# Performance work log

Measured on AMD Instinct MI355X. Metric: run time of the kernel, lower is better.

Reference implementation:

```python
import jax, jax.numpy as jnp
import numpy as np

M1 = M2 = M3 = 8  # retained modes per spatial dim


def get_3d_clifford_kernel(w, g):
    # w: (8, O, I, 2m1, 2m2, 2m3); returns (8O, 8I, 2m1, 2m2, 2m3)
    g0, g1, g2 = g[0], g[1], g[2]
    k0 = jnp.concatenate([w[0], w[1] * g0, w[2] * g1, w[3] * g2, -w[4] * g0 * g1, -w[5] * g0 * g2, -w[6] * g1 * g2, -w[7] * g0 * g1 * g2], axis=1)
    k1 = jnp.concatenate([w[1], w[0], -w[4] * g1, -w[5] * g2, w[2] * g1, w[3] * g2, -w[7] * g1 * g2, -w[6] * g1 * g2], axis=1)
    k2 = jnp.concatenate([w[2], w[4] * g0, w[0], -w[6] * g2, -w[1] * g0, w[7] * g0 * g2, w[3] * g2, w[5] * g0 * g2], axis=1)
    k3 = jnp.concatenate([w[3], w[5] * g0, w[6] * g1, w[0], -w[7] * g0 * g1, -w[1] * g0, -w[2] * g1, -w[4] * g0 * g1], axis=1)
    k4 = jnp.concatenate([w[4], w[2], -w[1], g2 * w[7], w[0], -w[6] * g2, w[5] * g2, w[3] * g2], axis=1)
    k5 = jnp.concatenate([w[5], w[3], -w[7] * g1, -w[1], w[6] * g1, w[0], -w[4] * g1, -w[2] * g1], axis=1)
    k6 = jnp.concatenate([w[6], w[7] * g0, w[3], -w[2], -w[5] * g0, w[4] * g0, w[0], w[1] * g0], axis=1)
    k7 = jnp.concatenate([w[7], w[6], -w[5], w[4], w[3], -w[2], w[1], w[0]], axis=1)
    return jnp.concatenate([k0, k1, k2, k3, k4, k5, k6, k7], axis=0)


def setup_inputs() -> dict:
    key = jax.random.key(0)
    k1, k2 = jax.random.split(key)
    B, D, H, W, Cin, Cout = 4, 48, 48, 48, 24, 24
    x = jax.random.normal(k1, (B, D, H, W, Cin, 8), dtype=jnp.float32)
    scale = 1.0 / (Cin * Cout)
    weights = scale * jax.random.uniform(k2, (8, Cout, Cin, 2 * M1, 2 * M2, 2 * M3), dtype=jnp.float32)
    return {"x": x, "weights": weights}


def reference(x, weights):
    B, D, H, W, Cin, _ = x.shape
    Cout = weights.shape[1]
    g = jnp.ones(3, dtype=x.dtype)  # metric (1, 1, 1)
    # complex-dual packing of the 8 blades
    d1 = x[..., 0] + 1j * x[..., 7]
    d2 = x[..., 1] + 1j * x[..., 6]
    d3 = x[..., 2] + 1j * x[..., 5]
    d4 = x[..., 3] + 1j * x[..., 4]
    f1 = jnp.fft.fftn(d1, axes=(1, 2, 3))
    f2 = jnp.fft.fftn(d2, axes=(1, 2, 3))
    f3 = jnp.fft.fftn(d3, axes=(1, 2, 3))
    f4 = jnp.fft.fftn(d4, axes=(1, 2, 3))
    bchw = lambda t: t.transpose(0, 4, 1, 2, 3)
    # (B, 8*Cin, D, H, W) real tensor of blade spectra
    mv_ft = jnp.concatenate([bchw(f1.real), bchw(f2.real), bchw(f3.real), bchw(f4.real),
                             bchw(f4.imag), bchw(f3.imag), bchw(f2.imag), bchw(f1.imag)], axis=1)
    # gather the 8 low/high-frequency octant corners -> (B, 8Cin, 2m1, 2m2, 2m3)
    i1 = jnp.concatenate([jnp.arange(M1), jnp.arange(D - M1, D)])
    i2 = jnp.concatenate([jnp.arange(M2), jnp.arange(H - M2, H)])
    i3 = jnp.concatenate([jnp.arange(M3), jnp.arange(W - M3, W)])
    input_mul = mv_ft[:, :, i1[:, None, None], i2[None, :, None], i3[None, None, :]]
    kernel = get_3d_clifford_kernel(weights, g)  # (8Cout, 8Cin, 2m1, 2m2, 2m3)
    output_mul = jnp.einsum("bixyz,oixyz->boxyz", input_mul, kernel)
    # scatter back to full spectrum
    out_ft = jnp.zeros((B, 8 * Cout, D, H, W), dtype=mv_ft.dtype)
    out_ft = out_ft.at[:, :, i1[:, None, None], i2[None, :, None], i3[None, None, :]].set(output_mul)
    out_ft = out_ft.reshape(B, 8, Cout, D, H, W).transpose(0, 2, 3, 4, 5, 1)  # (B, Cout, D, H, W, 8)
    o1 = out_ft[..., 0] + 1j * out_ft[..., 7]
    o2 = out_ft[..., 1] + 1j * out_ft[..., 6]
    o3 = out_ft[..., 2] + 1j * out_ft[..., 5]
    o4 = out_ft[..., 3] + 1j * out_ft[..., 4]
    g1_ = jnp.fft.ifftn(o1, axes=(2, 3, 4))
    g2_ = jnp.fft.ifftn(o2, axes=(2, 3, 4))
    g3_ = jnp.fft.ifftn(o3, axes=(2, 3, 4))
    g4_ = jnp.fft.ifftn(o4, axes=(2, 3, 4))
    output = jnp.stack([g1_.real, g2_.real, g3_.real, g4_.real,
                        g4_.imag, g3_.imag, g2_.imag, g1_.imag], axis=-1)  # (B, Cout, D, H, W, 8)
    return output.transpose(0, 2, 3, 4, 1, 5)  # (B, D, H, W, Cout, 8)
```

## Files before the change

kernel.cpp:

```cpp
#include <hip/hip_runtime.h>
#include <math.h>


#define C866 0.8660254037844386f

constexpr float FC0[8] = {1.0f, 0.99144486137885f, 0.96592582628907f, 0.92387953251129f,
                          0.86602540378444f, 0.79335334029124f, 0.70710678118655f, 0.60876142900872f};
constexpr float FS0[8] = {0.0f, 0.13052619222005f, 0.25881904510252f, 0.38268343236509f,
                          0.5f, 0.60876142900872f, 0.70710678118655f, 0.79335334029124f};
constexpr float FC1[8] = {0.5f, 0.60876142900872f, 0.70710678118655f, 0.79335334029124f,
                          0.86602540378444f, 0.92387953251129f, 0.96592582628907f, 0.99144486137885f};
constexpr float FS1[8] = {-0.86602540378444f, -0.79335334029124f, -0.70710678118655f, -0.60876142900872f,
                          -0.5f, -0.38268343236509f, -0.25881904510252f, -0.13052619222005f};

__device__ __forceinline__ uint32_t c2h(float2 z) {
  union { _Float16 h[2]; uint32_t u; } v;
  v.h[0] = (_Float16)z.x; v.h[1] = (_Float16)z.y;
  return v.u;
}
__device__ __forceinline__ float2 h2c(uint32_t u) {
  union { uint32_t u; _Float16 h[2]; } v;
  v.u = u;
  return make_float2((float)v.h[0], (float)v.h[1]);
}

__device__ __forceinline__ float2 cmul(float2 a, float2 b) {
  return make_float2(fmaf(a.x, b.x, -(a.y * b.y)), fmaf(a.x, b.y, a.y * b.x));
}
__device__ __forceinline__ void cfma(float2& acc, float2 a, float2 t) {
  acc.x = fmaf(a.x, t.x, acc.x); acc.x = fmaf(-a.y, t.y, acc.x);
  acc.y = fmaf(a.x, t.y, acc.y); acc.y = fmaf(a.y, t.x, acc.y);
}

struct FwdState {
  float2 acc[8], t[8], stp[8];
  float2 R1, R2;
};

__device__ __forceinline__ void fwd_init(FwdState& st, int half) {
#pragma unroll
  for (int r = 0; r < 8; ++r) {
    st.acc[r] = make_float2(0.f, 0.f);
    st.t[r] = make_float2(1.f, 0.f);
    st.stp[r] = make_float2(half ? FC1[r] : FC0[r],
                            half ? -FS1[r] : -FS0[r]);
  }
  st.R1 = half ? make_float2(-0.5f, -C866) : make_float2(1.f, 0.f);
  st.R2 = half ? make_float2(-0.5f,  C866) : make_float2(1.f, 0.f);
}

__device__ __forceinline__ void fwd_stepf(FwdState& st, float2 z0, float2 z1, float2 z2) {
  z1 = cmul(z1, st.R1);
  z2 = cmul(z2, st.R2);
  const float sx = z1.x + z2.x, sy = z1.y + z2.y;
  const float dx = z1.x - z2.x, dy = z1.y - z2.y;
  const float2 y0 = make_float2(z0.x + sx, z0.y + sy);
  const float tx = fmaf(-0.5f, sx, z0.x), ty = fmaf(-0.5f, sy, z0.y);
  const float ex = C866 * dx, ey = C866 * dy;
  const float2 y1 = make_float2(tx + ey, ty - ex);
  const float2 y2 = make_float2(tx - ey, ty + ex);
#pragma unroll
  for (int r = 0; r < 8; ++r) {
    const float2 yy = (r % 3 == 0) ? y0 : ((r % 3 == 1) ? y1 : y2);
    cfma(st.acc[r], yy, st.t[r]);
    st.t[r] = cmul(st.t[r], st.stp[r]);
  }
}

struct InvState {
  float2 zr[16], t[16];
};

__device__ __forceinline__ void inv_init(InvState& st) {
#pragma unroll
  for (int m = 0; m < 16; ++m) st.t[m] = make_float2(1.f, 0.f);
}

__device__ __forceinline__ void inv_stepf(InvState& st, float2& o0, float2& o1, float2& o2) {
  constexpr int JG[16] = {0,1,2,0,1,2,0,1, 1,2,0,1,2,0,1,2};
  float2 u0 = make_float2(0.f, 0.f), u1 = u0, u2 = u0;
#pragma unroll
  for (int m = 0; m < 16; ++m) {
    float2& uu = (JG[m] == 0) ? u0 : ((JG[m] == 1) ? u1 : u2);
    cfma(uu, st.zr[m], st.t[m]);
    const float2 stp = (m < 8) ? make_float2(FC0[m], FS0[m])
                               : make_float2(FC1[m - 8], FS1[m - 8]);
    st.t[m] = cmul(st.t[m], stp);
  }
  const float sx = u1.x + u2.x, sy = u1.y + u2.y;
  const float dx = u1.x - u2.x, dy = u1.y - u2.y;
  o0 = make_float2(u0.x + sx, u0.y + sy);
  const float tx = fmaf(-0.5f, sx, u0.x), ty = fmaf(-0.5f, sy, u0.y);
  const float ex = C866 * dx, ey = C866 * dy;
  o1 = make_float2(tx - ey, ty + ex);
  o2 = make_float2(tx + ey, ty - ex);
}

__global__ __launch_bounds__(192) void k_fwd_w(const float* __restrict__ x,
                                               uint32_t* __restrict__ A) {
  __shared__ __align__(16) uint32_t xs[48 * 96];
  {
    const float* xp = x + (size_t)blockIdx.x * 9216;
    for (int idx = threadIdx.x; idx < 1152; idx += 192) {
      const int w = idx / 24, ci = idx % 24;
      const float4 u = *(const float4*)(xp + w * 192 + ci * 8);
      const float4 v = *(const float4*)(xp + w * 192 + ci * 8 + 4);
      uint4 d;
      d.x = c2h(make_float2(u.x, v.w));
      d.y = c2h(make_float2(u.y, v.z));
      d.z = c2h(make_float2(u.z, v.y));
      d.w = c2h(make_float2(u.w, v.x));
      *(uint4*)(&xs[w * 96 + ci * 4]) = d;
    }
  }
  __syncthreads();

  const int q = threadIdx.x % 96, half = threadIdx.x / 96;
  FwdState st;
  fwd_init(st, half);
#pragma unroll 4
  for (int j = 0; j < 16; ++j) {
    const float2 z0 = h2c(xs[j * 96 + q]);
    const float2 z1 = h2c(xs[(j + 16) * 96 + q]);
    const float2 z2 = h2c(xs[(j + 32) * 96 + q]);
    fwd_stepf(st, z0, z1, z2);
  }
  const int bd = blockIdx.x / 48, h = blockIdx.x % 48;
  uint32_t* Ap = A + (((size_t)bd * 16 + half * 8) * 48 + h) * 96 + q;
#pragma unroll
  for (int r = 0; r < 8; ++r) Ap[(size_t)r * 4608] = c2h(st.acc[r]);
}

__global__ __launch_bounds__(192) void k_fwd_h(const uint32_t* __restrict__ A,
                                               uint32_t* __restrict__ Bv) {
  const int k3 = blockIdx.x & 15, bd = blockIdx.x >> 4;
  const int q = threadIdx.x % 96, half = threadIdx.x / 96;
  const uint32_t* Ap = A + ((size_t)bd * 16 + k3) * 4608 + q;
  FwdState st;
  fwd_init(st, half);
#pragma unroll 4
  for (int j = 0; j < 16; ++j) {
    const float2 z0 = h2c(Ap[j * 96]);
    const float2 z1 = h2c(Ap[(j + 16) * 96]);
    const float2 z2 = h2c(Ap[(j + 32) * 96]);
    fwd_stepf(st, z0, z1, z2);
  }
  const int b = bd / 48, d = bd % 48;
  uint32_t* Bp = Bv + (((size_t)b * 256 + half * 8 * 16 + k3) * 48 + d) * 96 + q;
#pragma unroll
  for (int r = 0; r < 8; ++r) Bp[(size_t)r * 73728] = c2h(st.acc[r]);
}

__global__ __launch_bounds__(192) void k_fwd_d(const uint32_t* __restrict__ Bv,
                                               uint32_t* __restrict__ Cv) {
  const int k23 = blockIdx.x & 255, b = blockIdx.x >> 8;
  const int q = threadIdx.x % 96, half = threadIdx.x / 96;
  const uint32_t* Bp = Bv + ((size_t)b * 256 + k23) * 4608 + q;
  FwdState st;
  fwd_init(st, half);
#pragma unroll 4
  for (int j = 0; j < 16; ++j) {
    const float2 z0 = h2c(Bp[j * 96]);
    const float2 z1 = h2c(Bp[(j + 16) * 96]);
    const float2 z2 = h2c(Bp[(j + 32) * 96]);
    fwd_stepf(st, z0, z1, z2);
  }
  uint32_t* Cp = Cv + ((size_t)b * 4096 + k23) * 96 + q;
#pragma unroll
  for (int r = 0; r < 8; ++r) Cp[(size_t)(half * 8 + r) * 24576] = c2h(st.acc[r]);
}

__global__ __launch_bounds__(256) void k_einsum(const uint32_t* __restrict__ Cv,
                                                const float* __restrict__ wgt,
                                                uint32_t* __restrict__ OMz) {
  const int mode = blockIdx.x * 64 + (threadIdx.x & 63);
  const int co = blockIdx.y * 4 + (threadIdx.x >> 6);
  const int cih = blockIdx.z;

  constexpr int WIDX[8][8] = {
      {0, 1, 2, 3, 4, 5, 6, 7}, {1, 0, 4, 5, 2, 3, 7, 6},
      {2, 4, 0, 6, 1, 7, 3, 5}, {3, 5, 6, 0, 7, 1, 2, 4},
      {4, 2, 1, 7, 0, 6, 5, 3}, {5, 3, 7, 1, 6, 0, 4, 2},
      {6, 7, 3, 2, 5, 4, 0, 1}, {7, 6, 5, 4, 3, 2, 1, 0}};
  constexpr int SGN[8][8] = {
      {1, 1, 1, 1, -1, -1, -1, -1}, {1, 1, -1, -1, 1, 1, -1, -1},
      {1, 1, 1, -1, -1, 1, 1, 1},   {1, 1, 1, 1, -1, -1, -1, -1},
      {1, 1, -1, 1, 1, -1, 1, 1},   {1, 1, -1, -1, 1, 1, -1, -1},
      {1, 1, 1, -1, -1, 1, 1, 1},   {1, 1, -1, 1, 1, -1, 1, 1}};

  float acc[8][4];
#pragma unroll
  for (int bo = 0; bo < 8; ++bo)
#pragma unroll
    for (int b = 0; b < 4; ++b) acc[bo][b] = 0.f;

#pragma unroll 2
  for (int cc = 0; cc < 12; ++cc) {
    const int ci = cih * 12 + cc;
    float w8[8];
#pragma unroll
    for (int k = 0; k < 8; ++k)
      w8[k] = wgt[(size_t)((k * 24 + co) * 24 + ci) * 4096 + mode];
#pragma unroll
    for (int b = 0; b < 4; ++b) {
      const uint4 U = *(const uint4*)(Cv + ((size_t)(b * 4096 + mode) * 96 + ci * 4));
      const float2 z0 = h2c(U.x), z1 = h2c(U.y), z2 = h2c(U.z), z3 = h2c(U.w);
      const float inv[8] = {z0.x, z1.x, z2.x, z3.x, z3.y, z2.y, z1.y, z0.y};
#pragma unroll
      for (int bo = 0; bo < 8; ++bo) {
#pragma unroll
        for (int bi = 0; bi < 8; ++bi) {
          const float wv = w8[WIDX[bo][bi]];
          if (SGN[bo][bi] > 0)
            acc[bo][b] = fmaf(wv, inv[bi], acc[bo][b]);
          else
            acc[bo][b] = fmaf(wv, -inv[bi], acc[bo][b]);
        }
      }
    }
  }
  uint32_t* OMp = OMz + (size_t)cih * 1572864;
#pragma unroll
  for (int b = 0; b < 4; ++b) {
    uint4 P;
    P.x = c2h(make_float2(acc[0][b], acc[7][b]));
    P.y = c2h(make_float2(acc[1][b], acc[6][b]));
    P.z = c2h(make_float2(acc[2][b], acc[5][b]));
    P.w = c2h(make_float2(acc[3][b], acc[4][b]));
    *(uint4*)(OMp + ((size_t)(b * 4096 + mode) * 96 + co * 4)) = P;
  }
}

__global__ __launch_bounds__(192) void k_inv_d(const uint32_t* __restrict__ OMz,
                                               uint32_t* __restrict__ IS1) {
  const int col = blockIdx.x * 2 + threadIdx.x / 96;
  const int q = threadIdx.x % 96;
  const int k23 = col & 255, b = col >> 8;
  const int k2 = k23 >> 4, k3 = k23 & 15;
  InvState st;
#pragma unroll
  for (int m = 0; m < 16; ++m) {
    const size_t idx = ((size_t)b * 4096 + m * 256 + k23) * 96 + q;
    const float2 pa = h2c(OMz[idx]);
    const float2 pb = h2c(OMz[idx + 1572864]);
    st.zr[m] = make_float2(pa.x + pb.x, pa.y + pb.y);
  }
  inv_init(st);
  uint32_t* Op = IS1 + ((size_t)b * 12288 + k3 * 16 + k2) * 96 + q;
#pragma unroll 2
  for (int j = 0; j < 16; ++j) {
    float2 o0, o1, o2;
    inv_stepf(st, o0, o1, o2);
    Op[(size_t)j * 24576] = c2h(o0);
    Op[(size_t)(j + 16) * 24576] = c2h(o1);
    Op[(size_t)(j + 32) * 24576] = c2h(o2);
  }
}

__global__ __launch_bounds__(192) void k_inv_h(const uint32_t* __restrict__ IS1,
                                               uint32_t* __restrict__ IS2) {
  const int col = blockIdx.x * 2 + threadIdx.x / 96;
  const int q = threadIdx.x % 96;
  const int m3 = col & 15, bd = col >> 4;
  const uint32_t* Ip = IS1 + ((size_t)bd * 256 + m3 * 16) * 96 + q;
  InvState st;
#pragma unroll
  for (int m = 0; m < 16; ++m) st.zr[m] = h2c(Ip[m * 96]);
  inv_init(st);
  uint32_t* Op = IS2 + ((size_t)bd * 768 + m3) * 96 + q;
#pragma unroll 2
  for (int j = 0; j < 16; ++j) {
    float2 o0, o1, o2;
    inv_stepf(st, o0, o1, o2);
    Op[(size_t)j * 1536] = c2h(o0);
    Op[(size_t)(j + 16) * 1536] = c2h(o1);
    Op[(size_t)(j + 32) * 1536] = c2h(o2);
  }
}

__global__ __launch_bounds__(192) void k_inv_w(const uint32_t* __restrict__ IS2,
                                               float* __restrict__ out) {
  const int blk = blockIdx.x * 2 + threadIdx.x / 96;
  const int q = threadIdx.x % 96;
  const int co = q >> 2, c = q & 3;
  const float norm = 1.0f / 110592.0f;
  InvState st;
#pragma unroll
  for (int m = 0; m < 16; ++m) {
    float2 z = h2c(IS2[((size_t)blk * 16 + m) * 96 + q]);
    st.zr[m] = make_float2(z.x * norm, z.y * norm);
  }
  inv_init(st);
  float* ob = out + (size_t)blk * 9216 + co * 8;
#pragma unroll 2
  for (int j = 0; j < 16; ++j) {
    float2 o0, o1, o2;
    inv_stepf(st, o0, o1, o2);
    float* p0 = ob + (size_t)j * 192;
    float* p1 = ob + (size_t)(j + 16) * 192;
    float* p2 = ob + (size_t)(j + 32) * 192;
    p0[c] = o0.x; p0[7 - c] = o0.y;
    p1[c] = o1.x; p1[7 - c] = o1.y;
    p2[c] = o2.x; p2[7 - c] = o2.y;
  }
}

extern "C" void kernel_launch(void* const* d_in, const int* in_sizes, int n_in,
                              void* d_out, int out_size, void* d_ws, size_t ws_size,
                              hipStream_t stream) {
  (void)in_sizes; (void)n_in; (void)out_size; (void)ws_size;
  const float* x = (const float*)d_in[0];
  const float* wgt = (const float*)d_in[1];
  float* out = (float*)d_out;

  char* ob = (char*)d_out;
  uint32_t* A   = (uint32_t*)(ob + 0);
  uint32_t* Bv  = (uint32_t*)(ob + 56623104);
  uint32_t* Cv  = (uint32_t*)(ob + 75497472);
  uint32_t* OMz = (uint32_t*)(ob + 81788928);
  uint32_t* IS1 = (uint32_t*)(ob + 0);
  uint32_t* IS2 = (uint32_t*)d_ws;

  k_fwd_w<<<9216, 192, 0, stream>>>(x, A);
  k_fwd_h<<<3072, 192, 0, stream>>>(A, Bv);
  k_fwd_d<<<1024, 192, 0, stream>>>(Bv, Cv);
  k_einsum<<<dim3(64, 6, 2), 256, 0, stream>>>(Cv, wgt, OMz);
  k_inv_d<<<512, 192, 0, stream>>>(OMz, IS1);
  k_inv_h<<<1536, 192, 0, stream>>>(IS1, IS2);
  k_inv_w<<<4608, 192, 0, stream>>>(IS2, out);
}
```

Baseline: 309.5 us.

## Fuse inverse H and W FFT passes through shared memory

Merges the inverse H-axis and W-axis FFT kernels into one kernel. The H-pass results for a (b,d) slice and a group of 24 channels are kept in LDS instead of going through a global intermediate, and the W-pass then reads them from LDS. This removes one global write/read round trip of the half-precision intermediate and one kernel launch. In exchange it uses about 75KB of LDS per block, which lowers occupancy, and the grid shrinks to 768 blocks of 384 threads. IS1 now lives in the workspace rather than the output buffer.

```diff
diff --git a/kernel.cpp b/kernel.cpp
--- a/kernel.cpp
+++ b/kernel.cpp
@@ -257,51 +257,58 @@
   }
 }
 
-__global__ __launch_bounds__(192) void k_inv_h(const uint32_t* __restrict__ IS1,
-                                               uint32_t* __restrict__ IS2) {
-  const int col = blockIdx.x * 2 + threadIdx.x / 96;
-  const int q = threadIdx.x % 96;
-  const int m3 = col & 15, bd = col >> 4;
-  const uint32_t* Ip = IS1 + ((size_t)bd * 256 + m3 * 16) * 96 + q;
-  InvState st;
-#pragma unroll
-  for (int m = 0; m < 16; ++m) st.zr[m] = h2c(Ip[m * 96]);
-  inv_init(st);
-  uint32_t* Op = IS2 + ((size_t)bd * 768 + m3) * 96 + q;
+__global__ __launch_bounds__(384) void k_inv_hw(const uint32_t* __restrict__ IS1,
+                                                float* __restrict__ out) {
+  __shared__ uint32_t sb[48 * 392];
+  const int bd = blockIdx.x, qg = blockIdx.y;
+  const int tid = threadIdx.x;
+  const int ql = tid % 24;
+  const int q = qg * 24 + ql;
+
+  {
+    const int m3 = tid / 24;
+    const uint32_t* Ip = IS1 + ((size_t)bd * 256 + m3 * 16) * 96 + q;
+    InvState st;
+#pragma unroll
+    for (int m2 = 0; m2 < 16; ++m2) st.zr[m2] = h2c(Ip[m2 * 96]);
+    inv_init(st);
+    uint32_t* sp = &sb[m3 * 24 + ql];
 #pragma unroll 2
-  for (int j = 0; j < 16; ++j) {
-    float2 o0, o1, o2;
-    inv_stepf(st, o0, o1, o2);
-    Op[(size_t)j * 1536] = c2h(o0);
-    Op[(size_t)(j + 16) * 1536] = c2h(o1);
-    Op[(size_t)(j + 32) * 1536] = c2h(o2);
-  }
-}
-
-__global__ __launch_bounds__(192) void k_inv_w(const uint32_t* __restrict__ IS2,
-                                               float* __restrict__ out) {
-  const int blk = blockIdx.x * 2 + threadIdx.x / 96;
-  const int q = threadIdx.x % 96;
-  const int co = q >> 2, c = q & 3;
-  const float norm = 1.0f / 110592.0f;
-  InvState st;
-#pragma unroll
-  for (int m = 0; m < 16; ++m) {
-    float2 z = h2c(IS2[((size_t)blk * 16 + m) * 96 + q]);
-    st.zr[m] = make_float2(z.x * norm, z.y * norm);
-  }
-  inv_init(st);
-  float* ob = out + (size_t)blk * 9216 + co * 8;
+    for (int j = 0; j < 16; ++j) {
+      float2 o0, o1, o2;
+      inv_stepf(st, o0, o1, o2);
+      sp[(size_t)j * 392] = c2h(o0);
+      sp[(size_t)(j + 16) * 392] = c2h(o1);
+      sp[(size_t)(j + 32) * 392] = c2h(o2);
+    }
+  }
+  __syncthreads();
+  {
+    const int co = q >> 2, c = q & 3;
+    const float norm = 1.0f / 110592.0f;
+    for (int hh = 0; hh < 3; ++hh) {
+      const int h = hh * 16 + tid / 24;
+      const uint32_t* sp = &sb[h * 392 + ql];
+      InvState st;
+#pragma unroll
+      for (int m3 = 0; m3 < 16; ++m3) {
+        const float2 z = h2c(sp[m3 * 24]);
+        st.zr[m3] = make_float2(z.x * norm, z.y * norm);
+      }
+      inv_init(st);
+      float* ob = out + (((size_t)bd * 48 + h) * 48) * 192 + co * 8;
 #pragma unroll 2
-  for (int j = 0; j < 16; ++j) {
-    float2 o0, o1, o2;
-    inv_stepf(st, o0, o1, o2);
-    float* p0 = ob + (size_t)j * 192;
-    float* p1 = ob + (size_t)(j + 16) * 192;
-    float* p2 = ob + (size_t)(j + 32) * 192;
-    p0[c] = o0.x; p0[7 - c] = o0.y;
-    p1[c] = o1.x; p1[7 - c] = o1.y;
-    p2[c] = o2.x; p2[7 - c] = o2.y;
+      for (int j = 0; j < 16; ++j) {
+        float2 o0, o1, o2;
+        inv_stepf(st, o0, o1, o2);
+        float* p0 = ob + (size_t)j * 192;
+        float* p1 = ob + (size_t)(j + 16) * 192;
+        float* p2 = ob + (size_t)(j + 32) * 192;
+        p0[c] = o0.x; p0[7 - c] = o0.y;
+        p1[c] = o1.x; p1[7 - c] = o1.y;
+        p2[c] = o2.x; p2[7 - c] = o2.y;
+      }
+    }
   }
 }
 
@@ -318,14 +325,12 @@
   uint32_t* Bv  = (uint32_t*)(ob + 56623104);
   uint32_t* Cv  = (uint32_t*)(ob + 75497472);
   uint32_t* OMz = (uint32_t*)(ob + 81788928);
-  uint32_t* IS1 = (uint32_t*)(ob + 0);
-  uint32_t* IS2 = (uint32_t*)d_ws;
+  uint32_t* IS1 = (uint32_t*)d_ws;
 
   k_fwd_w<<<9216, 192, 0, stream>>>(x, A);
   k_fwd_h<<<3072, 192, 0, stream>>>(A, Bv);
   k_fwd_d<<<1024, 192, 0, stream>>>(Bv, Cv);
   k_einsum<<<dim3(64, 6, 2), 256, 0, stream>>>(Cv, wgt, OMz);
   k_inv_d<<<512, 192, 0, stream>>>(OMz, IS1);
-  k_inv_h<<<1536, 192, 0, stream>>>(IS1, IS2);
-  k_inv_w<<<4608, 192, 0, stream>>>(IS2, out);
-}
+  k_inv_hw<<<dim3(192, 4), 384, 0, stream>>>(IS1, out);
+}
```

Measured after the change: 320.7 us. 3.6% more time.
